# Optimization experiments

Measured on AMD Instinct MI355X. Metric: run time of the kernel, lower is better.

Reference implementation:

```python
import jax, jax.numpy as jnp
import numpy as np
from jax import lax

BLOCK_SIZE = 5
GAMMA = 0.02


def setup_inputs() -> dict:
    key = jax.random.key(0)
    kx, km = jax.random.split(key)
    N, C, H, W = 64, 64, 80, 80
    x = jax.random.normal(kx, (N, C, H, W), dtype=jnp.float32)
    # Bernoulli(gamma) sample, materialized as an int32 0/1 mask (the module's
    # internal randomness, fixed for deterministic reference comparison).
    mask = (jax.random.uniform(km, (N, C, H, W)) < GAMMA).astype(jnp.int32)
    return {"x": x, "mask": mask}


def _dropblock(x, mask, block_size):
    m = mask.astype(x.dtype)  # 0/1 seed mask, shape (N,C,H,W)
    # Original scatters each seed (h,w) into [h, h+bs) x [w, w+bs) (clipped at
    # H,W). Equivalent dense form: block_mask[i,j] = max over m[i-dh, j-dw],
    # dh,dw in [0,bs) -> sliding-window max with top/left padding of bs-1.
    if block_size > 1:
        block_mask = lax.reduce_window(
            m,
            jnp.array(0.0, x.dtype),
            lax.max,
            window_dimensions=(1, 1, block_size, block_size),
            window_strides=(1, 1, 1, 1),
            padding=((0, 0), (0, 0), (block_size - 1, 0), (block_size - 1, 0)),
        )
    else:
        block_mask = m
    inv_blk_mask = 1.0 - block_mask
    countM = jnp.array(m.size, x.dtype)
    count_ones = inv_blk_mask.sum()
    return inv_blk_mask * x * (countM / count_ones)


def reference(x, mask):
    return _dropblock(x, mask, BLOCK_SIZE)
```

## Files before the change

kernel.cpp:

```cpp
#include <hip/hip_runtime.h>

#define DB_H 80
#define DB_W 80
#define DB_PLANE (DB_H * DB_W)
#define DB_NPLANES 4096
#define DB_TOTAL (DB_PLANE * DB_NPLANES)
#define DB_COUNT_F 26214400.0f
#define DB_CNT_BYTES (DB_NPLANES * 4)
#define DB_BP_UINT4 (DB_NPLANES * DB_H)
#define WPB 4

__global__ __launch_bounds__(256) void db_mask_bp(
    const int4* __restrict__ mask4,
    uint4* __restrict__ bp,
    unsigned int* __restrict__ counts)
{
    __shared__ unsigned long long G[WPB][26 * 4];
    __shared__ unsigned int RO[WPB][DB_H * 4];
    const int wid = threadIdx.x >> 6, lane = threadIdx.x & 63;
    const int plane = blockIdx.x * WPB + wid;
    const int4* mp = mask4 + plane * (DB_PLANE / 4);
    unsigned long long* Gp = G[wid];
    unsigned int* ro = RO[wid];

    if (lane < 4) Gp[25 * 4 + lane] = 0ULL;

    #pragma unroll 1
    for (int c = 0; c < 5; ++c) {
        int4 v[5];
        #pragma unroll
        for (int k = 0; k < 5; ++k) v[k] = mp[(c * 5 + k) * 64 + lane];
        #pragma unroll
        for (int k = 0; k < 5; ++k) {
            unsigned long long b0 = __ballot(v[k].x & 1);
            unsigned long long b1 = __ballot(v[k].y & 1);
            unsigned long long b2 = __ballot(v[k].z & 1);
            unsigned long long b3 = __ballot(v[k].w & 1);
            if (lane < 4) {
                unsigned long long bw =
                    (lane == 0) ? b0 : (lane == 1) ? b1 : (lane == 2) ? b2 : b3;
                Gp[(c * 5 + k) * 4 + lane] = bw;
            }
        }
    }

    #pragma unroll 1
    for (int rr = 0; rr < 2; ++rr) {
        const int r = rr * 64 + lane;
        if (r < DB_H) {
            const int e0 = r * DB_W;
            const int g = e0 >> 8;
            const int l0 = (e0 & 255) >> 2;
            const unsigned long long* Gw = Gp + g * 4;
            const bool cross = l0 > 44;
            const int sh = 64 - l0;
            unsigned long long s;
            unsigned p0, p1, p2, p3;
            s = Gw[0] >> l0; if (cross) s |= Gw[4] << sh; p0 = (unsigned)s & 0xFFFFF;
            s = Gw[1] >> l0; if (cross) s |= Gw[5] << sh; p1 = (unsigned)s & 0xFFFFF;
            s = Gw[2] >> l0; if (cross) s |= Gw[6] << sh; p2 = (unsigned)s & 0xFFFFF;
            s = Gw[3] >> l0; if (cross) s |= Gw[7] << sh; p3 = (unsigned)s & 0xFFFFF;
            const unsigned q23 = p2 | p3, q123 = p1 | q23, t = p0 | q123;
            const unsigned a01 = p0 | p1, a012 = a01 | p2;
            const unsigned r0 = (p0   | (t    << 1)) & 0xFFFFF;
            const unsigned r1 = (a01  | (q123 << 1)) & 0xFFFFF;
            const unsigned r2 = (a012 | (q23  << 1)) & 0xFFFFF;
            const unsigned r3 = (t    | (p3   << 1)) & 0xFFFFF;
            ((uint4*)ro)[r] = make_uint4(r0, r1, r2, r3);
        }
    }

    unsigned int zeros = 0;
    #pragma unroll 1
    for (int rr = 0; rr < 2; ++rr) {
        const int i = rr * 64 + lane;
        if (i < DB_H) {
            const int lo = (i >= 4) ? i - 4 : 0;
            unsigned c0 = 0, c1 = 0, c2 = 0, c3 = 0;
            for (int ii = lo; ii <= i; ++ii) {
                const uint4 rv = ((const uint4*)ro)[ii];
                c0 |= rv.x; c1 |= rv.y; c2 |= rv.z; c3 |= rv.w;
            }
            zeros += 80u - __popc(c0) - __popc(c1) - __popc(c2) - __popc(c3);
            bp[plane * DB_H + i] = make_uint4(c0, c1, c2, c3);
        }
    }
    for (int off = 32; off > 0; off >>= 1)
        zeros += (unsigned int)__shfl_down((int)zeros, off, 64);
    if (lane == 0) counts[plane] = zeros;
}

__global__ __launch_bounds__(256) void db_apply_bp(
    const float4* __restrict__ x,
    const uint4* __restrict__ bp,
    const unsigned int* __restrict__ counts,
    float4* __restrict__ out)
{
    __shared__ float s_scale;
    __shared__ unsigned int s_part[4];
    {
        const uint4* cp = (const uint4*)counts;
        unsigned int c = 0;
        #pragma unroll
        for (int k = 0; k < 4; ++k) {
            uint4 v = cp[k * 256 + threadIdx.x];
            c += v.x + v.y + v.z + v.w;
        }
        for (int off = 32; off > 0; off >>= 1)
            c += (unsigned int)__shfl_down((int)c, off, 64);
        if ((threadIdx.x & 63) == 0) s_part[threadIdx.x >> 6] = c;
        __syncthreads();
        if (threadIdx.x == 0)
            s_scale = DB_COUNT_F /
                      (float)(s_part[0] + s_part[1] + s_part[2] + s_part[3]);
        __syncthreads();
    }
    const float scale = s_scale;
    const unsigned NG = DB_TOTAL / 4;
    const unsigned stride = gridDim.x * blockDim.x;
    #pragma unroll 2
    for (unsigned g = blockIdx.x * blockDim.x + threadIdx.x; g < NG; g += stride) {
        const unsigned plane = g / 1600u;
        const unsigned gp = g - plane * 1600u;
        const unsigned i = gp / 20u;
        const unsigned l = gp - i * 20u;
        const uint4 b = bp[plane * DB_H + i];
        const float4 v = x[g];
        float4 o;
        o.x = ((b.x >> l) & 1u) ? 0.0f : v.x * scale;
        o.y = ((b.y >> l) & 1u) ? 0.0f : v.y * scale;
        o.z = ((b.z >> l) & 1u) ? 0.0f : v.z * scale;
        o.w = ((b.w >> l) & 1u) ? 0.0f : v.w * scale;
        out[g] = o;
    }
}

__global__ __launch_bounds__(256) void db_count_kernel(
    const int* __restrict__ mask,
    unsigned int* __restrict__ counts)
{
    __shared__ unsigned long long P[WPB][104];
    __shared__ unsigned int RO[WPB][DB_H * 3];
    const int wid = threadIdx.x >> 6, lane = threadIdx.x & 63;
    const int plane = blockIdx.x * WPB + wid;
    const int* mp = mask + plane * DB_PLANE;
    unsigned long long* Pp = P[wid];
    unsigned int* ro = RO[wid];
    #pragma unroll 1
    for (int c = 0; c < 10; ++c) {
        int v[10];
        #pragma unroll
        for (int k = 0; k < 10; ++k) v[k] = mp[(c * 10 + k) * 64 + lane];
        #pragma unroll
        for (int k = 0; k < 10; ++k) {
            unsigned long long bal = __ballot(v[k] & 1);
            if (lane == 0) Pp[c * 10 + k] = bal;
        }
    }
    if (lane < 4) Pp[100 + lane] = 0ULL;
    __syncthreads();
    for (int r = lane; r < DB_H; r += 64) {
        const int bitpos = r * DB_W;
        const int q = bitpos >> 6, off = bitpos & 63;
        unsigned long long a, b;
        if (off) {
            a = (Pp[q] >> off) | (Pp[q + 1] << (64 - off));
            b = (Pp[q + 1] >> off) | (Pp[q + 2] << (64 - off));
        } else {
            a = Pp[q]; b = Pp[q + 1];
        }
        b &= 0xFFFFULL;
        unsigned long long ra = a, rb = b;
        #pragma unroll
        for (int s = 1; s <= 4; ++s) {
            ra |= a << s;
            rb |= (b << s) | (a >> (64 - s));
        }
        rb &= 0xFFFFULL;
        ro[r * 3 + 0] = (unsigned int)ra;
        ro[r * 3 + 1] = (unsigned int)(ra >> 32);
        ro[r * 3 + 2] = (unsigned int)rb;
    }
    __syncthreads();
    unsigned int zeros = 0;
    for (int i = lane; i < DB_H; i += 64) {
        const int lo = (i >= 4) ? i - 4 : 0;
        unsigned int c0 = 0, c1 = 0, c2 = 0;
        for (int ii = lo; ii <= i; ++ii) {
            c0 |= ro[ii * 3 + 0];
            c1 |= ro[ii * 3 + 1];
            c2 |= ro[ii * 3 + 2];
        }
        zeros += 80u - __popc(c0) - __popc(c1) - __popc(c2);
    }
    for (int off = 32; off > 0; off >>= 1)
        zeros += (unsigned int)__shfl_down((int)zeros, off, 64);
    if (lane == 0) counts[plane] = zeros;
}

__global__ __launch_bounds__(256) void db_apply_recompute(
    const float* __restrict__ x,
    const int* __restrict__ mask,
    const unsigned int* __restrict__ counts,
    float* __restrict__ out)
{
    __shared__ unsigned long long P[WPB][104];
    __shared__ unsigned int RO[WPB][DB_H * 3];
    __shared__ unsigned int BM[WPB][DB_H * 3];
    __shared__ float s_scale;
    __shared__ unsigned int s_part[4];
    {
        const uint4* cp = (const uint4*)counts;
        unsigned int c = 0;
        #pragma unroll
        for (int k = 0; k < 4; ++k) {
            uint4 v = cp[k * 256 + threadIdx.x];
            c += v.x + v.y + v.z + v.w;
        }
        for (int off = 32; off > 0; off >>= 1)
            c += (unsigned int)__shfl_down((int)c, off, 64);
        if ((threadIdx.x & 63) == 0) s_part[threadIdx.x >> 6] = c;
        __syncthreads();
        if (threadIdx.x == 0)
            s_scale = DB_COUNT_F /
                      (float)(s_part[0] + s_part[1] + s_part[2] + s_part[3]);
        __syncthreads();
    }
    const float scale = s_scale;
    const int wid = threadIdx.x >> 6, lane = threadIdx.x & 63;
    const int plane = blockIdx.x * WPB + wid;
    const int* mp = mask + plane * DB_PLANE;
    unsigned long long* Pp = P[wid];
    unsigned int* ro = RO[wid];
    #pragma unroll 1
    for (int c = 0; c < 10; ++c) {
        int v[10];
        #pragma unroll
        for (int k = 0; k < 10; ++k) v[k] = mp[(c * 10 + k) * 64 + lane];
        #pragma unroll
        for (int k = 0; k < 10; ++k) {
            unsigned long long bal = __ballot(v[k] & 1);
            if (lane == 0) Pp[c * 10 + k] = bal;
        }
    }
    if (lane < 4) Pp[100 + lane] = 0ULL;
    __syncthreads();
    for (int r = lane; r < DB_H; r += 64) {
        const int bitpos = r * DB_W;
        const int q = bitpos >> 6, off = bitpos & 63;
        unsigned long long a, b;
        if (off) {
            a = (Pp[q] >> off) | (Pp[q + 1] << (64 - off));
            b = (Pp[q + 1] >> off) | (Pp[q + 2] << (64 - off));
        } else {
            a = Pp[q]; b = Pp[q + 1];
        }
        b &= 0xFFFFULL;
        unsigned long long ra = a, rb = b;
        #pragma unroll
        for (int s = 1; s <= 4; ++s) {
            ra |= a << s;
            rb |= (b << s) | (a >> (64 - s));
        }
        rb &= 0xFFFFULL;
        ro[r * 3 + 0] = (unsigned int)ra;
        ro[r * 3 + 1] = (unsigned int)(ra >> 32);
        ro[r * 3 + 2] = (unsigned int)rb;
    }
    __syncthreads();
    unsigned int* bmp = BM[wid];
    for (int i = lane; i < DB_H; i += 64) {
        const int lo = (i >= 4) ? i - 4 : 0;
        unsigned int c0 = 0, c1 = 0, c2 = 0;
        for (int ii = lo; ii <= i; ++ii) {
            c0 |= ro[ii * 3 + 0];
            c1 |= ro[ii * 3 + 1];
            c2 |= ro[ii * 3 + 2];
        }
        bmp[i * 3 + 0] = c0; bmp[i * 3 + 1] = c1; bmp[i * 3 + 2] = c2;
    }
    __syncthreads();
    const float* xp = x + plane * DB_PLANE;
    float* op = out + plane * DB_PLANE;
    for (int e = lane; e < DB_PLANE; e += 64) {
        int i = e / DB_W, j = e - i * DB_W;
        unsigned int wb = bmp[i * 3 + (j >> 5)] >> (j & 31);
        op[e] = (wb & 1u) ? 0.0f : xp[e] * scale;
    }
}

extern "C" void kernel_launch(void* const* d_in, const int* in_sizes, int n_in,
                              void* d_out, int out_size, void* d_ws, size_t ws_size,
                              hipStream_t stream) {
    const float* x = (const float*)d_in[0];
    const int* mask = (const int*)d_in[1];
    float* out = (float*)d_out;

    unsigned int* counts = (unsigned int*)d_ws;
    uint4* bp = (uint4*)((char*)d_ws + DB_CNT_BYTES);
    const size_t need = DB_CNT_BYTES + (size_t)DB_BP_UINT4 * sizeof(uint4);

    if (ws_size >= need) {
        db_mask_bp<<<DB_NPLANES / WPB, 256, 0, stream>>>(
            (const int4*)mask, bp, counts);
        db_apply_bp<<<2048, 256, 0, stream>>>(
            (const float4*)x, bp, counts, (float4*)out);
    } else {
        db_count_kernel<<<DB_NPLANES / WPB, 256, 0, stream>>>(mask, counts);
        db_apply_recompute<<<DB_NPLANES / WPB, 256, 0, stream>>>(
            x, mask, counts, out);
    }
}
```

Measured before the change: 68.02 us.

## Build row-major block mask per lane with shuffles and skip fully masked x loads

The mask kernel now has each lane read one contiguous 80-int row, pack it into three 32-bit words, do the horizontal dilation in registers and the vertical dilation with cross-lane shuffles. This replaces the ballot/LDS phase-split bitmap and the shared-memory row-OR passes. The apply kernel reads the block mask as row-major nibbles and skips loading x when all four elements are dropped. The trade-off is uncoalesced per-lane strided mask reads (lanes are 320 bytes apart) and a second pass with only 20 active lanes for the tail rows.

Result: slower. 69.57 us (+2.3%).

```diff
diff --git a/kernel.cpp b/kernel.cpp
--- a/kernel.cpp
+++ b/kernel.cpp
@@ -10,87 +10,121 @@
 #define DB_BP_UINT4 (DB_NPLANES * DB_H)
 #define WPB 4
 
-__global__ __launch_bounds__(256) void db_mask_bp(
+__global__ __launch_bounds__(256, 4) void db_mask_rows(
     const int4* __restrict__ mask4,
     uint4* __restrict__ bp,
     unsigned int* __restrict__ counts)
 {
-    __shared__ unsigned long long G[WPB][26 * 4];
-    __shared__ unsigned int RO[WPB][DB_H * 4];
     const int wid = threadIdx.x >> 6, lane = threadIdx.x & 63;
     const int plane = blockIdx.x * WPB + wid;
-    const int4* mp = mask4 + plane * (DB_PLANE / 4);
-    unsigned long long* Gp = G[wid];
-    unsigned int* ro = RO[wid];
-
-    if (lane < 4) Gp[25 * 4 + lane] = 0ULL;
-
-    #pragma unroll 1
-    for (int c = 0; c < 5; ++c) {
-        int4 v[5];
-        #pragma unroll
-        for (int k = 0; k < 5; ++k) v[k] = mp[(c * 5 + k) * 64 + lane];
-        #pragma unroll
-        for (int k = 0; k < 5; ++k) {
-            unsigned long long b0 = __ballot(v[k].x & 1);
-            unsigned long long b1 = __ballot(v[k].y & 1);
-            unsigned long long b2 = __ballot(v[k].z & 1);
-            unsigned long long b3 = __ballot(v[k].w & 1);
-            if (lane < 4) {
-                unsigned long long bw =
-                    (lane == 0) ? b0 : (lane == 1) ? b1 : (lane == 2) ? b2 : b3;
-                Gp[(c * 5 + k) * 4 + lane] = bw;
-            }
-        }
-    }
-
-    #pragma unroll 1
-    for (int rr = 0; rr < 2; ++rr) {
-        const int r = rr * 64 + lane;
-        if (r < DB_H) {
-            const int e0 = r * DB_W;
-            const int g = e0 >> 8;
-            const int l0 = (e0 & 255) >> 2;
-            const unsigned long long* Gw = Gp + g * 4;
-            const bool cross = l0 > 44;
-            const int sh = 64 - l0;
-            unsigned long long s;
-            unsigned p0, p1, p2, p3;
-            s = Gw[0] >> l0; if (cross) s |= Gw[4] << sh; p0 = (unsigned)s & 0xFFFFF;
-            s = Gw[1] >> l0; if (cross) s |= Gw[5] << sh; p1 = (unsigned)s & 0xFFFFF;
-            s = Gw[2] >> l0; if (cross) s |= Gw[6] << sh; p2 = (unsigned)s & 0xFFFFF;
-            s = Gw[3] >> l0; if (cross) s |= Gw[7] << sh; p3 = (unsigned)s & 0xFFFFF;
-            const unsigned q23 = p2 | p3, q123 = p1 | q23, t = p0 | q123;
-            const unsigned a01 = p0 | p1, a012 = a01 | p2;
-            const unsigned r0 = (p0   | (t    << 1)) & 0xFFFFF;
-            const unsigned r1 = (a01  | (q123 << 1)) & 0xFFFFF;
-            const unsigned r2 = (a012 | (q23  << 1)) & 0xFFFFF;
-            const unsigned r3 = (t    | (p3   << 1)) & 0xFFFFF;
-            ((uint4*)ro)[r] = make_uint4(r0, r1, r2, r3);
-        }
-    }
+    const int4* mp = mask4 + (size_t)plane * 1600;
 
     unsigned int zeros = 0;
-    #pragma unroll 1
-    for (int rr = 0; rr < 2; ++rr) {
-        const int i = rr * 64 + lane;
-        if (i < DB_H) {
-            const int lo = (i >= 4) ? i - 4 : 0;
-            unsigned c0 = 0, c1 = 0, c2 = 0, c3 = 0;
-            for (int ii = lo; ii <= i; ++ii) {
-                const uint4 rv = ((const uint4*)ro)[ii];
-                c0 |= rv.x; c1 |= rv.y; c2 |= rv.z; c3 |= rv.w;
-            }
-            zeros += 80u - __popc(c0) - __popc(c1) - __popc(c2) - __popc(c3);
-            bp[plane * DB_H + i] = make_uint4(c0, c1, c2, c3);
-        }
-    }
+
+    {
+        const int4* rp = mp + lane * 20;
+        unsigned b0 = 0, b1 = 0, b2 = 0;
+        int4 v[10];
+        #pragma unroll
+        for (int k = 0; k < 10; ++k) v[k] = rp[k];
+        #pragma unroll
+        for (int k = 0; k < 10; ++k) {
+            const unsigned nib = (unsigned)(v[k].x & 1) |
+                                 ((unsigned)(v[k].y & 1) << 1) |
+                                 ((unsigned)(v[k].z & 1) << 2) |
+                                 ((unsigned)(v[k].w & 1) << 3);
+            if (k < 8) b0 |= nib << (k * 4);
+            else       b1 |= nib << ((k - 8) * 4);
+        }
+        #pragma unroll
+        for (int k = 0; k < 10; ++k) v[k] = rp[10 + k];
+        #pragma unroll
+        for (int k = 0; k < 10; ++k) {
+            const int kk = 10 + k;
+            const unsigned nib = (unsigned)(v[k].x & 1) |
+                                 ((unsigned)(v[k].y & 1) << 1) |
+                                 ((unsigned)(v[k].z & 1) << 2) |
+                                 ((unsigned)(v[k].w & 1) << 3);
+            if (kk < 16) b1 |= nib << ((kk - 8) * 4);
+            else         b2 |= nib << ((kk - 16) * 4);
+        }
+        unsigned r0 = b0, r1 = b1, r2 = b2;
+        #pragma unroll
+        for (int s = 1; s <= 4; ++s) {
+            r0 |= b0 << s;
+            r1 |= (b1 << s) | (b0 >> (32 - s));
+            r2 |= (b2 << s) | (b1 >> (32 - s));
+        }
+        r2 &= 0xFFFFu;
+        unsigned c0 = r0, c1 = r1, c2 = r2;
+        #pragma unroll
+        for (int k = 1; k <= 4; ++k) {
+            const int src = (lane >= k) ? (lane - k) : 0;
+            const unsigned s0 = (unsigned)__shfl((int)r0, src, 64);
+            const unsigned s1 = (unsigned)__shfl((int)r1, src, 64);
+            const unsigned s2 = (unsigned)__shfl((int)r2, src, 64);
+            if (lane >= k) { c0 |= s0; c1 |= s1; c2 |= s2; }
+        }
+        zeros += 80u - __popc(c0) - __popc(c1) - __popc(c2);
+        bp[(size_t)plane * DB_H + lane] = make_uint4(c0, c1, c2, 0u);
+    }
+
+    if (lane < 20) {
+        const int row = 60 + lane;
+        const int4* rp = mp + row * 20;
+        unsigned b0 = 0, b1 = 0, b2 = 0;
+        int4 v[10];
+        #pragma unroll
+        for (int k = 0; k < 10; ++k) v[k] = rp[k];
+        #pragma unroll
+        for (int k = 0; k < 10; ++k) {
+            const unsigned nib = (unsigned)(v[k].x & 1) |
+                                 ((unsigned)(v[k].y & 1) << 1) |
+                                 ((unsigned)(v[k].z & 1) << 2) |
+                                 ((unsigned)(v[k].w & 1) << 3);
+            if (k < 8) b0 |= nib << (k * 4);
+            else       b1 |= nib << ((k - 8) * 4);
+        }
+        #pragma unroll
+        for (int k = 0; k < 10; ++k) v[k] = rp[10 + k];
+        #pragma unroll
+        for (int k = 0; k < 10; ++k) {
+            const int kk = 10 + k;
+            const unsigned nib = (unsigned)(v[k].x & 1) |
+                                 ((unsigned)(v[k].y & 1) << 1) |
+                                 ((unsigned)(v[k].z & 1) << 2) |
+                                 ((unsigned)(v[k].w & 1) << 3);
+            if (kk < 16) b1 |= nib << ((kk - 8) * 4);
+            else         b2 |= nib << ((kk - 16) * 4);
+        }
+        unsigned r0 = b0, r1 = b1, r2 = b2;
+        #pragma unroll
+        for (int s = 1; s <= 4; ++s) {
+            r0 |= b0 << s;
+            r1 |= (b1 << s) | (b0 >> (32 - s));
+            r2 |= (b2 << s) | (b1 >> (32 - s));
+        }
+        r2 &= 0xFFFFu;
+        unsigned c0 = r0, c1 = r1, c2 = r2;
+        #pragma unroll
+        for (int k = 1; k <= 4; ++k) {
+            const unsigned s0 = (unsigned)__shfl((int)r0, lane - k, 64);
+            const unsigned s1 = (unsigned)__shfl((int)r1, lane - k, 64);
+            const unsigned s2 = (unsigned)__shfl((int)r2, lane - k, 64);
+            if (lane >= k) { c0 |= s0; c1 |= s1; c2 |= s2; }
+        }
+        if (lane >= 4) {
+            zeros += 80u - __popc(c0) - __popc(c1) - __popc(c2);
+            bp[(size_t)plane * DB_H + row] = make_uint4(c0, c1, c2, 0u);
+        }
+    }
+
     for (int off = 32; off > 0; off >>= 1)
         zeros += (unsigned int)__shfl_down((int)zeros, off, 64);
     if (lane == 0) counts[plane] = zeros;
 }
 
-__global__ __launch_bounds__(256) void db_apply_bp(
+__global__ __launch_bounds__(256) void db_apply_bits(
     const float4* __restrict__ x,
     const uint4* __restrict__ bp,
     const unsigned int* __restrict__ counts,
@@ -123,14 +157,17 @@
         const unsigned plane = g / 1600u;
         const unsigned gp = g - plane * 1600u;
         const unsigned i = gp / 20u;
-        const unsigned l = gp - i * 20u;
+        const unsigned q = gp - i * 20u;
         const uint4 b = bp[plane * DB_H + i];
-        const float4 v = x[g];
+        const unsigned word = (q < 8u) ? b.x : ((q < 16u) ? b.y : b.z);
+        const unsigned nib = (word >> ((q & 7u) * 4u)) & 0xFu;
+        float4 v = make_float4(0.f, 0.f, 0.f, 0.f);
+        if (nib != 0xFu) v = x[g];
         float4 o;
-        o.x = ((b.x >> l) & 1u) ? 0.0f : v.x * scale;
-        o.y = ((b.y >> l) & 1u) ? 0.0f : v.y * scale;
-        o.z = ((b.z >> l) & 1u) ? 0.0f : v.z * scale;
-        o.w = ((b.w >> l) & 1u) ? 0.0f : v.w * scale;
+        o.x = (nib & 1u) ? 0.0f : v.x * scale;
+        o.y = (nib & 2u) ? 0.0f : v.y * scale;
+        o.z = (nib & 4u) ? 0.0f : v.z * scale;
+        o.w = (nib & 8u) ? 0.0f : v.w * scale;
         out[g] = o;
     }
 }
@@ -301,9 +338,9 @@
     const size_t need = DB_CNT_BYTES + (size_t)DB_BP_UINT4 * sizeof(uint4);
 
     if (ws_size >= need) {
-        db_mask_bp<<<DB_NPLANES / WPB, 256, 0, stream>>>(
+        db_mask_rows<<<DB_NPLANES / WPB, 256, 0, stream>>>(
             (const int4*)mask, bp, counts);
-        db_apply_bp<<<2048, 256, 0, stream>>>(
+        db_apply_bits<<<2048, 256, 0, stream>>>(
             (const float4*)x, bp, counts, (float4*)out);
     } else {
         db_count_kernel<<<DB_NPLANES / WPB, 256, 0, stream>>>(mask, counts);
```
